# Kernel optimization log

Measured on AMD Instinct MI355X. Metric: run time of the kernel, lower is better.

The kernel has to match this reference:

```python
import jax, jax.numpy as jnp
import numpy as np

B, T, C, H, D = 4, 2048, 1024, 16, 64  # batch, seq, n_embd, n_head, head_size


def setup_inputs() -> dict:
    key = jax.random.key(0)
    ks = jax.random.split(key, 8)
    s = 0.02  # init scale for weights
    return {
        "q": jax.random.normal(ks[0], (B, T, C), jnp.float32),
        "k": jax.random.normal(ks[1], (B, T, C), jnp.float32),
        "v": jax.random.normal(ks[2], (B, T, C), jnp.float32),
        "Wq": jax.random.normal(ks[3], (H, C, D), jnp.float32) * s,
        "Wk": jax.random.normal(ks[4], (H, C, D), jnp.float32) * s,
        "Wv": jax.random.normal(ks[5], (H, C, D), jnp.float32) * s,
        "Wo": jax.random.normal(ks[6], (H * D, C), jnp.float32) * s,
        "bo": jnp.zeros((C,), jnp.float32),
    }


def reference(q, k, v, Wq, Wk, Wv, Wo, bo):
    # Per-head projections (vectorized over heads): [B,T,C] x [H,C,D] -> [B,H,T,D]
    qh = jnp.einsum('btc,hcd->bhtd', q, Wq)
    kh = jnp.einsum('btc,hcd->bhtd', k, Wk)
    vh = jnp.einsum('btc,hcd->bhtd', v, Wv)
    # NOTE: source divides by sqrt(C) = sqrt(n_embd), not sqrt(head_size)
    scale = 1.0 / jnp.sqrt(jnp.float32(C))
    att = jnp.einsum('bhtd,bhsd->bhts', qh, kh) * scale  # [B,H,T,T]
    causal = jnp.tril(jnp.ones((T, T), dtype=bool))
    att = jnp.where(causal, att, -jnp.inf)
    p = jax.nn.softmax(att, axis=-1)  # dropout is identity in eval mode
    out = jnp.einsum('bhts,bhsd->bhtd', p, vh)
    # concat heads in order: [B,H,T,D] -> [B,T,H*D]
    out = out.transpose(0, 2, 1, 3).reshape(B, T, H * D)
    return out @ Wo + bo
```

## Files before the change

### kernel.cpp

```cpp
#include <hip/hip_runtime.h>
#include <hip/hip_bf16.h>
#include <cstdint>
#include <cstddef>

#define B_  4
#define T_  2048
#define C_  1024
#define H_  16
#define D_  64
#define MROWS (B_*T_)
#define NDIM  (H_*D_)

typedef float  f32x4 __attribute__((ext_vector_type(4)));
typedef __bf16 bfrag __attribute__((ext_vector_type(8)));

__device__ __forceinline__ unsigned short f2bf(float f) {
  union { float f; unsigned u; } v; v.f = f;
  unsigned r = v.u + 0x7fffu + ((v.u >> 16) & 1u);
  return (unsigned short)(r >> 16);
}

__device__ __forceinline__ void async_load16(const void* g, void* l) {
  __builtin_amdgcn_global_load_lds((__attribute__((address_space(1))) void*)(void*)g,
                                   (__attribute__((address_space(3))) void*)l,
                                   16, 0, 0);
}

__device__ __forceinline__ unsigned pack_bf2(float f0, float f1) {
  unsigned a0 = __float_as_uint(f0) + 0x8000u;
  unsigned a1 = __float_as_uint(f1) + 0x8000u;
  return __builtin_amdgcn_perm(a1, a0, 0x07060302u);
}

__global__ __launch_bounds__(256) void prep_kernel(
    const float* __restrict__ q, const float* __restrict__ k, const float* __restrict__ v,
    unsigned short* __restrict__ qb, unsigned short* __restrict__ kb, unsigned short* __restrict__ vb,
    const float* __restrict__ Wq, const float* __restrict__ Wk, const float* __restrict__ Wv,
    unsigned short* __restrict__ wqT, unsigned short* __restrict__ wkT, unsigned short* __restrict__ wvT,
    const float* __restrict__ Wo, unsigned short* __restrict__ woT)
{
  const int id = blockIdx.x, tid = threadIdx.x;
  if (id < 24576) {
    int z = id >> 13, blk = id & 8191;
    const float* in = z == 0 ? q : z == 1 ? k : v;
    unsigned short* out = z == 0 ? qb : z == 1 ? kb : vb;
    int i = (blk * 256 + tid) * 4;
    float4 vv = *(const float4*)(in + i);
    ushort4 r;
    r.x = f2bf(vv.x); r.y = f2bf(vv.y); r.z = f2bf(vv.z); r.w = f2bf(vv.w);
    *(ushort4*)(out + i) = r;
  } else if (id < 25344) {
    int u = id - 24576;
    int z = u >> 4, cblk = u & 15;
    int sel = z >> 4, h = z & 15;
    const float* in = (sel == 0 ? Wq : sel == 1 ? Wk : Wv) + (size_t)h * C_ * D_;
    unsigned short* out = (sel == 0 ? wqT : sel == 1 ? wkT : wvT) + (size_t)h * D_ * C_;
    __shared__ float tile[64][65];
    int c0 = cblk * 64;
    int x = tid & 63, y4 = tid >> 6;
    for (int r = y4; r < 64; r += 4)
      tile[r][x] = in[(size_t)(c0 + r) * D_ + x];
    __syncthreads();
    for (int r = y4; r < 64; r += 4)
      out[(size_t)r * C_ + c0 + x] = f2bf(tile[x][r]);
  } else {
    int u = id - 25344;
    __shared__ float tile[64][65];
    int i0 = (u >> 4) * 64, j0 = (u & 15) * 64;
    int x = tid & 63, y4 = tid >> 6;
    for (int r = y4; r < 64; r += 4)
      tile[r][x] = Wo[(size_t)(i0 + r) * C_ + j0 + x];
    __syncthreads();
    for (int r = y4; r < 64; r += 4)
      woT[(size_t)(j0 + r) * NDIM + i0 + x] = f2bf(tile[x][r]);
  }
}

template <int EPI>
__global__ __launch_bounds__(256) void gemm_bt_kernel(
    const unsigned short* __restrict__ A0, const unsigned short* __restrict__ A1, const unsigned short* __restrict__ A2,
    const unsigned short* __restrict__ B0, const unsigned short* __restrict__ B1, const unsigned short* __restrict__ B2,
    void* C0, void* C1, void* C2, const float* __restrict__ bias,
    int M, int N, int K)
{
  const int id = blockIdx.x;
  const int xcd = id & 7, s = id >> 3;
  const int z = s >> 6;
  const int t = s & 63;
  const int mb = xcd * 8 + (t >> 3);
  const int nb = t & 7;

  const unsigned short* A  = z == 0 ? A0 : z == 1 ? A1 : A2;
  const unsigned short* Bt = z == 0 ? B0 : z == 1 ? B1 : B2;
  void* Cv                 = z == 0 ? C0 : z == 1 ? C1 : C2;

  __shared__ __align__(16) short As[128 * 64];
  __shared__ __align__(16) short Bs[128 * 64];

  const int tid = threadIdx.x, lane = tid & 63, wave = tid >> 6;
  const int quad = lane >> 4, l15 = lane & 15;
  const int m0 = mb * 128, n0 = nb * 128;
  const int wm = (wave >> 1) * 64, wn = (wave & 1) * 64;

  f32x4 acc[4][4] = {};

  for (int k0 = 0; k0 < K; k0 += 64) {
#pragma unroll
    for (int i = 0; i < 4; ++i) {
      int p0 = (wave * 4 + i) * 64;
      int p = p0 + lane;
      int m = p >> 3, cl = (p & 7) ^ (m & 7);
      async_load16(A  + (size_t)(m0 + m) * K + k0 + cl * 8, (char*)As + p0 * 16);
      async_load16(Bt + (size_t)(n0 + m) * K + k0 + cl * 8, (char*)Bs + p0 * 16);
    }
    __syncthreads();
#pragma unroll
    for (int ks = 0; ks < 2; ++ks) {
      bfrag af[4], bf[4];
#pragma unroll
      for (int i = 0; i < 4; ++i) {
        int m = wm + i * 16 + l15;
        int c = (ks * 4 + quad) ^ (m & 7);
        af[i] = *(const bfrag*)(As + m * 64 + c * 8);
        int n = wn + i * 16 + l15;
        int c2 = (ks * 4 + quad) ^ (n & 7);
        bf[i] = *(const bfrag*)(Bs + n * 64 + c2 * 8);
      }
#pragma unroll
      for (int i = 0; i < 4; ++i)
#pragma unroll
        for (int j = 0; j < 4; ++j)
          acc[i][j] = __builtin_amdgcn_mfma_f32_16x16x32_bf16(af[i], bf[j], acc[i][j], 0, 0, 0);
    }
    __syncthreads();
  }

  if constexpr (EPI == 0) {
    if (z < 2) {
      unsigned short* Cb = (unsigned short*)Cv;
#pragma unroll
      for (int i = 0; i < 4; ++i) {
        int row0 = m0 + wm + i * 16 + quad * 4;
#pragma unroll
        for (int j = 0; j < 4; ++j) {
          int col = n0 + wn + j * 16 + l15;
#pragma unroll
          for (int r = 0; r < 4; ++r)
            Cb[(size_t)(row0 + r) * N + col] = f2bf(acc[i][j][r]);
        }
      }
    } else {
      unsigned short* Vo = (unsigned short*)Cv;
#pragma unroll
      for (int i = 0; i < 4; ++i) {
        int m = m0 + wm + i * 16 + quad * 4;
        int bb = m >> 11, tt = m & 2047;
#pragma unroll
        for (int j = 0; j < 4; ++j) {
          int n = n0 + wn + j * 16 + l15;
          int hh = n >> 6, dd = n & 63;
          ushort4 pk;
          pk.x = f2bf(acc[i][j][0]); pk.y = f2bf(acc[i][j][1]);
          pk.z = f2bf(acc[i][j][2]); pk.w = f2bf(acc[i][j][3]);
          *(ushort4*)(Vo + (((size_t)bb * 16 + hh) * 64 + dd) * T_ + tt) = pk;
        }
      }
    }
  } else {
    float* Cf = (float*)Cv;
#pragma unroll
    for (int j = 0; j < 4; ++j) {
      int col = n0 + wn + j * 16 + l15;
      float bv = bias[col];
#pragma unroll
      for (int i = 0; i < 4; ++i) {
        int row0 = m0 + wm + i * 16 + quad * 4;
#pragma unroll
        for (int r = 0; r < 4; ++r)
          Cf[(size_t)(row0 + r) * N + col] = acc[i][j][r] + bv;
      }
    }
  }
}

__global__ __launch_bounds__(256, 3) void flash_kernel(
    const unsigned short* __restrict__ Qh, const unsigned short* __restrict__ Kh,
    const unsigned short* __restrict__ VT, unsigned short* __restrict__ Oh)
{
  __shared__ __align__(16) short Ks[128 * 64];
  __shared__ __align__(16) short Vt[2][64 * 64];
  __shared__ __align__(16) short Ps[4][32 * 72];

  const int tid = threadIdx.x, lane = tid & 63, wave = tid >> 6;
  const int quad = lane >> 4, l15 = lane & 15;
  const int id = blockIdx.x;
  const int rr = id >> 8, cc = id & 255, g = cc >> 6, bh = cc & 63;
  const int t = (rr == 0) ? g : (rr == 1) ? 7 - g : (rr == 2) ? 8 + g : 15 - g;
  const int b = bh >> 4, h = bh & 15;
  const int q0 = t * 128;

  const unsigned short* Qbase = Qh + (size_t)b * T_ * NDIM + h * 64;
  const unsigned short* Kbase = Kh + (size_t)b * T_ * NDIM + h * 64;
  const unsigned short* Vbase = VT + ((size_t)(b * 16 + h) * 64) * T_;

  const int wrow_lo = q0 + wave * 32;

  bfrag qfr[2][2];
#pragma unroll
  for (int j = 0; j < 2; ++j)
#pragma unroll
    for (int ks = 0; ks < 2; ++ks)
      qfr[j][ks] = *(const bfrag*)(Qbase + (size_t)(wrow_lo + j * 16 + l15) * NDIM + ks * 32 + quad * 8);

  float l_st[2] = {0.f, 0.f};
  f32x4 o_acc[2][4] = {};
  short* pw = &Ps[wave][0];
  const float c32 = 0.045084220f;

  for (int kv0 = 0; kv0 < q0 + 128; kv0 += 128) {
#pragma unroll
    for (int i = 0; i < 4; ++i) {
      int p0 = (wave * 4 + i) * 64;
      int p = p0 + lane;
      int kr = p >> 3, kcl = (p & 7) ^ (kr & 7);
      async_load16(Kbase + (size_t)(kv0 + kr) * NDIM + kcl * 8, (char*)Ks + p0 * 16);
      int hh = p >> 9, d = (p >> 3) & 63, vcl = (p & 7) ^ (d & 7);
      async_load16(Vbase + (size_t)d * T_ + kv0 + hh * 64 + vcl * 8, (char*)Vt + p0 * 16);
    }
    __syncthreads();

#pragma unroll
    for (int hf = 0; hf < 2; ++hf) {
      const int kvh = kv0 + hf * 64;
      if (kvh > wrow_lo + 31) break;

      f32x4 sv[2][4] = {};
#pragma unroll
      for (int ks = 0; ks < 2; ++ks) {
        bfrag kf[4];
#pragma unroll
        for (int i = 0; i < 4; ++i) {
          int key = i * 16 + l15;
          int c = (ks * 4 + quad) ^ (key & 7);
          kf[i] = *(const bfrag*)(Ks + (hf * 64 + key) * 64 + c * 8);
        }
#pragma unroll
        for (int j = 0; j < 2; ++j)
#pragma unroll
          for (int i = 0; i < 4; ++i)
            sv[j][i] = __builtin_amdgcn_mfma_f32_16x16x32_bf16(kf[i], qfr[j][ks], sv[j][i], 0, 0, 0);
      }

#pragma unroll
      for (int j = 0; j < 2; ++j)
#pragma unroll
        for (int i = 0; i < 4; ++i)
#pragma unroll
          for (int r = 0; r < 4; ++r)
            sv[j][i][r] = __builtin_amdgcn_exp2f(sv[j][i][r] * c32);
      if (kvh + 63 > wrow_lo) {
#pragma unroll
        for (int j = 0; j < 2; ++j) {
          int qr = wrow_lo + j * 16 + l15;
#pragma unroll
          for (int i = 0; i < 4; ++i) {
            int keyb = kvh + i * 16 + quad * 4;
#pragma unroll
            for (int r = 0; r < 4; ++r)
              if (keyb + r > qr) sv[j][i][r] = 0.f;
          }
        }
      }

#pragma unroll
      for (int j = 0; j < 2; ++j) {
#pragma unroll
        for (int i = 0; i < 4; ++i) {
          l_st[j] += sv[j][i][0] + sv[j][i][1] + sv[j][i][2] + sv[j][i][3];
          uint2 pk;
          pk.x = pack_bf2(sv[j][i][0], sv[j][i][1]);
          pk.y = pack_bf2(sv[j][i][2], sv[j][i][3]);
          *(uint2*)(pw + (j * 16 + l15) * 72 + i * 16 + quad * 4) = pk;
        }
      }

#pragma unroll
      for (int ks = 0; ks < 2; ++ks) {
        bfrag vf[4], pf[2];
#pragma unroll
        for (int i2 = 0; i2 < 4; ++i2) {
          int d = i2 * 16 + l15;
          int c = (ks * 4 + quad) ^ (d & 7);
          vf[i2] = *(const bfrag*)(&Vt[hf][0] + d * 64 + c * 8);
        }
#pragma unroll
        for (int j = 0; j < 2; ++j)
          pf[j] = *(const bfrag*)(pw + (j * 16 + l15) * 72 + ks * 32 + quad * 8);
#pragma unroll
        for (int j = 0; j < 2; ++j)
#pragma unroll
          for (int i2 = 0; i2 < 4; ++i2)
            o_acc[j][i2] = __builtin_amdgcn_mfma_f32_16x16x32_bf16(vf[i2], pf[j], o_acc[j][i2], 0, 0, 0);
      }
    }
    __syncthreads();
  }

#pragma unroll
  for (int j = 0; j < 2; ++j) {
    float s = l_st[j];
    s += __shfl_xor(s, 16, 64);
    s += __shfl_xor(s, 32, 64);
    float inv = 1.f / s;
    int qr = q0 + wave * 32 + j * 16 + l15;
    size_t base = ((size_t)b * T_ + qr) * NDIM + h * 64;
#pragma unroll
    for (int i2 = 0; i2 < 4; ++i2) {
      ushort4 pk;
      pk.x = f2bf(o_acc[j][i2][0] * inv);
      pk.y = f2bf(o_acc[j][i2][1] * inv);
      pk.z = f2bf(o_acc[j][i2][2] * inv);
      pk.w = f2bf(o_acc[j][i2][3] * inv);
      *(ushort4*)(Oh + base + i2 * 16 + quad * 4) = pk;
    }
  }
}

extern "C" void kernel_launch(void* const* d_in, const int* in_sizes, int n_in,
                              void* d_out, int out_size, void* d_ws, size_t ws_size,
                              hipStream_t stream)
{
  const float* q  = (const float*)d_in[0];
  const float* k  = (const float*)d_in[1];
  const float* v  = (const float*)d_in[2];
  const float* Wq = (const float*)d_in[3];
  const float* Wk = (const float*)d_in[4];
  const float* Wv = (const float*)d_in[5];
  const float* Wo = (const float*)d_in[6];
  const float* bo = (const float*)d_in[7];
  float* out = (float*)d_out;

  char* w = (char*)d_ws;
  const size_t szBTC = (size_t)MROWS * C_ * 2;
  const size_t szW   = (size_t)NDIM * C_ * 2;
  unsigned short* qb   = (unsigned short*)(w);
  unsigned short* kb   = (unsigned short*)(w + szBTC);
  unsigned short* vb   = (unsigned short*)(w + 2 * szBTC);
  unsigned short* wqT  = (unsigned short*)(w + 3 * szBTC);
  unsigned short* wkT  = (unsigned short*)(w + 3 * szBTC + szW);
  unsigned short* wvT  = (unsigned short*)(w + 3 * szBTC + 2 * szW);
  unsigned short* woT  = (unsigned short*)(w + 3 * szBTC + 3 * szW);
  unsigned short* qhp  = (unsigned short*)(w + 3 * szBTC + 4 * szW);
  unsigned short* khp  = (unsigned short*)(w + 4 * szBTC + 4 * szW);
  unsigned short* vT   = (unsigned short*)(w + 5 * szBTC + 4 * szW);
  unsigned short* attO = (unsigned short*)(w + 6 * szBTC + 4 * szW);

  prep_kernel<<<dim3(25600), 256, 0, stream>>>(q, k, v, qb, kb, vb,
                                               Wq, Wk, Wv, wqT, wkT, wvT, Wo, woT);

  gemm_bt_kernel<0><<<dim3(1536), 256, 0, stream>>>(
      qb, kb, vb, wqT, wkT, wvT, qhp, khp, vT, nullptr, MROWS, NDIM, C_);

  flash_kernel<<<dim3(1024), 256, 0, stream>>>(qhp, khp, vT, attO);

  gemm_bt_kernel<1><<<dim3(512), 256, 0, stream>>>(
      attO, attO, attO, woT, woT, woT, out, out, out, bo, MROWS, C_, NDIM);
}
```

Measured before the change: 302.0 us.

## Replace QKV projection GEMM with 256x256-tile 8-wave ping-pong pipelined kernel

Adds a dedicated QKV projection GEMM that uses 256x256 output tiles with 512 threads, double-buffered async global-to-LDS loads, and an XOR-swizzled LDS layout. The K loop is split into quarter-phases, each with barriers and raised scheduling priority around the MFMA blocks, so loads for the next stage overlap compute. Larger tiles increase operand reuse and cut global traffic. The trade-off is a grid of only 384 blocks and a heavy per-thread register load.

```diff
diff --git a/kernel.cpp b/kernel.cpp
--- a/kernel.cpp
+++ b/kernel.cpp
@@ -76,6 +76,192 @@
   }
 }
 
+__global__ __launch_bounds__(512, 2) void gemm_qkv_256(
+    const unsigned short* __restrict__ A0, const unsigned short* __restrict__ A1, const unsigned short* __restrict__ A2,
+    const unsigned short* __restrict__ B0t, const unsigned short* __restrict__ B1t, const unsigned short* __restrict__ B2t,
+    void* C0, void* C1, void* C2)
+{
+  constexpr int K = C_;
+  constexpr int N = NDIM;
+  __shared__ __align__(16) short As[2 * 16384];
+  __shared__ __align__(16) short Bs[2 * 16384];
+
+  const int id = blockIdx.x;
+  const int xcd = id & 7, s = id >> 3;
+  const int z = s >> 4, t = s & 15;
+  const int mb = xcd * 4 + (t >> 2), nb = t & 3;
+  const int m0 = mb * 256, n0 = nb * 256;
+
+  const unsigned short* A  = z == 0 ? A0 : z == 1 ? A1 : A2;
+  const unsigned short* Bt = z == 0 ? B0t : z == 1 ? B1t : B2t;
+
+  const int tid = threadIdx.x, lane = tid & 63;
+  const int quad = lane >> 4, l15 = lane & 15;
+  const int wave = tid >> 6;
+  const int qr = wave >> 2, qc = wave & 3;
+  const int wbase = tid & ~63;
+
+  f32x4 acc[2][2][4][2] = {};
+
+  auto stageA = [&](int buf, int kt, int h) {
+#pragma unroll
+    for (int i2 = 0; i2 < 2; ++i2) {
+      int p0 = h * 1024 + i2 * 512 + wbase;
+      int p  = p0 + lane;
+      int m  = p >> 3, cl = (p & 7) ^ (m & 7);
+      async_load16(A + (size_t)(m0 + m) * K + kt * 64 + cl * 8,
+                   (char*)As + buf * 32768 + p0 * 16);
+    }
+  };
+  auto stageB = [&](int buf, int kt, int h) {
+#pragma unroll
+    for (int i2 = 0; i2 < 2; ++i2) {
+      int p0 = h * 1024 + i2 * 512 + wbase;
+      int p  = p0 + lane;
+      int m  = p >> 3, cl = (p & 7) ^ (m & 7);
+      async_load16(Bt + (size_t)(n0 + m) * K + kt * 64 + cl * 8,
+                   (char*)Bs + buf * 32768 + p0 * 16);
+    }
+  };
+
+  bfrag a[2][4];
+  bfrag b[2][2];
+  bfrag b2[2][2];
+
+  auto ldA = [&](int buf, int QR) {
+#pragma unroll
+    for (int ks = 0; ks < 2; ++ks)
+#pragma unroll
+      for (int i = 0; i < 4; ++i) {
+        int row = QR * 128 + qr * 64 + i * 16 + l15;
+        int c = (ks * 4 + quad) ^ (row & 7);
+        a[ks][i] = *(const bfrag*)(As + buf * 16384 + row * 64 + c * 8);
+      }
+  };
+  auto ldB = [&](bfrag (&bb)[2][2], int buf, int QC) {
+#pragma unroll
+    for (int ks = 0; ks < 2; ++ks)
+#pragma unroll
+      for (int j = 0; j < 2; ++j) {
+        int col = QC * 128 + qc * 32 + j * 16 + l15;
+        int c = (ks * 4 + quad) ^ (col & 7);
+        bb[ks][j] = *(const bfrag*)(Bs + buf * 16384 + col * 64 + c * 8);
+      }
+  };
+  auto mm = [&](f32x4 (&ac)[4][2], bfrag (&bb)[2][2]) {
+    __builtin_amdgcn_s_setprio(1);
+#pragma unroll
+    for (int ks = 0; ks < 2; ++ks)
+#pragma unroll
+      for (int i = 0; i < 4; ++i)
+#pragma unroll
+        for (int j = 0; j < 2; ++j)
+          ac[i][j] = __builtin_amdgcn_mfma_f32_16x16x32_bf16(a[ks][i], bb[ks][j], ac[i][j], 0, 0, 0);
+    __builtin_amdgcn_s_setprio(0);
+  };
+
+#define PH_BAR() __builtin_amdgcn_s_barrier()
+#define PH_LGK() asm volatile("s_waitcnt lgkmcnt(0)" ::: "memory")
+
+  stageA(0, 0, 0); stageB(0, 0, 0);
+  stageA(0, 0, 1); stageB(0, 0, 1);
+  stageA(1, 1, 0); stageB(1, 1, 0);
+  asm volatile("s_waitcnt vmcnt(4)" ::: "memory");
+  PH_BAR();
+
+#pragma unroll 1
+  for (int k0 = 0; k0 <= 12; k0 += 2) {
+    ldA(0, 0); ldB(b, 0, 0);
+    stageA(1, k0 + 1, 1);
+    PH_BAR(); PH_LGK(); mm(acc[0][0], b); PH_BAR();
+    ldB(b2, 0, 1);
+    stageB(1, k0 + 1, 1);
+    PH_BAR(); PH_LGK(); mm(acc[0][1], b2); PH_BAR();
+    ldA(0, 1);
+    stageA(0, k0 + 2, 0);
+    PH_BAR(); PH_LGK(); mm(acc[1][0], b); PH_BAR();
+    stageB(0, k0 + 2, 0);
+    PH_BAR(); PH_LGK(); mm(acc[1][1], b2);
+    asm volatile("s_waitcnt vmcnt(4)" ::: "memory");
+    PH_BAR();
+    ldA(1, 0); ldB(b, 1, 0);
+    stageA(0, k0 + 2, 1);
+    PH_BAR(); PH_LGK(); mm(acc[0][0], b); PH_BAR();
+    ldB(b2, 1, 1);
+    stageB(0, k0 + 2, 1);
+    PH_BAR(); PH_LGK(); mm(acc[0][1], b2); PH_BAR();
+    ldA(1, 1);
+    stageA(1, k0 + 3, 0);
+    PH_BAR(); PH_LGK(); mm(acc[1][0], b); PH_BAR();
+    stageB(1, k0 + 3, 0);
+    PH_BAR(); PH_LGK(); mm(acc[1][1], b2);
+    asm volatile("s_waitcnt vmcnt(4)" ::: "memory");
+    PH_BAR();
+  }
+
+  ldA(0, 0); ldB(b, 0, 0);
+  stageA(1, 15, 1);
+  PH_BAR(); PH_LGK(); mm(acc[0][0], b); PH_BAR();
+  ldB(b2, 0, 1);
+  stageB(1, 15, 1);
+  PH_BAR(); PH_LGK(); mm(acc[0][1], b2); PH_BAR();
+  ldA(0, 1);
+  PH_BAR(); PH_LGK(); mm(acc[1][0], b); PH_BAR();
+  PH_BAR(); PH_LGK(); mm(acc[1][1], b2);
+  asm volatile("s_waitcnt vmcnt(0)" ::: "memory");
+  PH_BAR();
+  ldA(1, 0); ldB(b, 1, 0);
+  PH_BAR(); PH_LGK(); mm(acc[0][0], b); PH_BAR();
+  ldB(b2, 1, 1);
+  PH_BAR(); PH_LGK(); mm(acc[0][1], b2); PH_BAR();
+  ldA(1, 1);
+  PH_BAR(); PH_LGK(); mm(acc[1][0], b); PH_BAR();
+  PH_LGK(); mm(acc[1][1], b2);
+
+#undef PH_BAR
+#undef PH_LGK
+
+  void* Cv = z == 0 ? C0 : z == 1 ? C1 : C2;
+  if (z < 2) {
+    unsigned short* Cb = (unsigned short*)Cv;
+#pragma unroll
+    for (int QR = 0; QR < 2; ++QR)
+#pragma unroll
+      for (int QC = 0; QC < 2; ++QC)
+#pragma unroll
+        for (int i = 0; i < 4; ++i) {
+          int row0 = m0 + QR * 128 + qr * 64 + i * 16 + quad * 4;
+#pragma unroll
+          for (int j = 0; j < 2; ++j) {
+            int col = n0 + QC * 128 + qc * 32 + j * 16 + l15;
+#pragma unroll
+            for (int r = 0; r < 4; ++r)
+              Cb[(size_t)(row0 + r) * N + col] = f2bf(acc[QR][QC][i][j][r]);
+          }
+        }
+  } else {
+    unsigned short* Vo = (unsigned short*)Cv;
+#pragma unroll
+    for (int QR = 0; QR < 2; ++QR)
+#pragma unroll
+      for (int QC = 0; QC < 2; ++QC)
+#pragma unroll
+        for (int i = 0; i < 4; ++i) {
+          int m = m0 + QR * 128 + qr * 64 + i * 16 + quad * 4;
+          int bb = m >> 11, tt = m & 2047;
+#pragma unroll
+          for (int j = 0; j < 2; ++j) {
+            int n = n0 + QC * 128 + qc * 32 + j * 16 + l15;
+            int hh = n >> 6, dd = n & 63;
+            ushort4 pk;
+            pk.x = f2bf(acc[QR][QC][i][j][0]); pk.y = f2bf(acc[QR][QC][i][j][1]);
+            pk.z = f2bf(acc[QR][QC][i][j][2]); pk.w = f2bf(acc[QR][QC][i][j][3]);
+            *(ushort4*)(Vo + (((size_t)bb * 16 + hh) * 64 + dd) * T_ + tt) = pk;
+          }
+        }
+  }
+}
+
 template <int EPI>
 __global__ __launch_bounds__(256) void gemm_bt_kernel(
     const unsigned short* __restrict__ A0, const unsigned short* __restrict__ A1, const unsigned short* __restrict__ A2,
@@ -358,8 +544,8 @@
   prep_kernel<<<dim3(25600), 256, 0, stream>>>(q, k, v, qb, kb, vb,
                                                Wq, Wk, Wv, wqT, wkT, wvT, Wo, woT);
 
-  gemm_bt_kernel<0><<<dim3(1536), 256, 0, stream>>>(
-      qb, kb, vb, wqT, wkT, wvT, qhp, khp, vT, nullptr, MROWS, NDIM, C_);
+  gemm_qkv_256<<<dim3(384), 512, 0, stream>>>(
+      qb, kb, vb, wqT, wkT, wvT, qhp, khp, vT);
 
   flash_kernel<<<dim3(1024), 256, 0, stream>>>(qhp, khp, vT, attO);
 
```

Measured after the change: 305.8 us. Within noise of the previous version (+1.3%).
